# Performance work log

Hardware: AMD Instinct MI355X
Metric: run time of the kernel (lower is better)

The kernel has to match this reference:

```python
import jax, jax.numpy as jnp
import numpy as np

G = 128          # dense grid extent per axis
N = 131072       # number of occupied voxels
MUL = 32         # multiplicity of 0e and 1o irreps
DIM = 4 * MUL    # 32 scalars + 32 vectors*3 = 128
NB = 5           # num_radial_basis
R = 2.5          # diameter / 2
K = 125          # 5^3 kernel offsets


def _lattice_constants():
    # 5x5x5 lattice of physical offsets (steps = 1.0)
    v = jnp.arange(-2.0, 3.0)
    xx, yy, zz = jnp.meshgrid(v, v, v, indexing='ij')
    lattice = jnp.stack([xx, yy, zz], -1)              # (5,5,5,3)
    norm = jnp.linalg.norm(lattice, axis=-1)           # (5,5,5)
    # soft_one_hot_linspace, basis='smooth_finite', cutoff=True
    values = jnp.linspace(0.0, R, NB + 2)[1:-1]
    step = R / (NB + 1)
    d = (norm[..., None] - values) / step              # (5,5,5,NB)
    inside = jnp.abs(d) < 1.0
    ds = jnp.clip(d, -1.0 + 1e-6, 1.0 - 1e-6)
    emb = jnp.where(inside, 1.14136 * jnp.exp(2.0 - 1.0 / (1.0 + ds) - 1.0 / (1.0 - ds)), 0.0)
    # spherical harmonics l=0,1, normalize=True, 'component' norm (e3nn l=1 order: y,z,x)
    unit = jnp.where(norm[..., None] > 0, lattice / jnp.maximum(norm, 1e-9)[..., None], 0.0)
    Y0 = jnp.ones_like(norm)
    Y1 = jnp.sqrt(3.0) * unit[..., (1, 2, 0)]          # (5,5,5,3)
    return emb, Y0, Y1


def _kernel(weight):
    """Generate the (125, DIM, DIM) equivariant kernel (tp.right analogue)."""
    emb, Y0, Y1 = _lattice_constants()
    w = (emb @ weight) / K                              # (5,5,5,4096), /= 5*5*5
    w = w.reshape(5, 5, 5, 4, MUL, MUL)
    Wa, Wb, Wc, Wd = w[..., 0, :, :], w[..., 1, :, :], w[..., 2, :, :], w[..., 3, :, :]
    c = 1.0 / jnp.sqrt(64.0)   # path norm: fan = 2 paths * 32*1 per output
    # 0e x 0e -> 0e
    Kss = c * Wa * Y0[..., None, None]                                        # (...,u,w)
    # 0e x 1o -> 1o  (w3j 1/sqrt3 * sqrt(dim_out=3) = 1)
    Ksv = c * jnp.einsum('...uw,...k->...uwk', Wb, Y1).reshape(5, 5, 5, MUL, 3 * MUL)
    # 1o x 1o -> 0e  (dot / sqrt3)
    Kvs = (c / jnp.sqrt(3.0)) * jnp.einsum('...uw,...i->...uiw', Wd, Y1).reshape(5, 5, 5, 3 * MUL, MUL)
    # 1o x 0e -> 1o  (identity on the 3-vector)
    Kvv = c * jnp.einsum('...uw,ik->...uiwk', Wc * Y0[..., None, None], jnp.eye(3)).reshape(5, 5, 5, 3 * MUL, 3 * MUL)
    kern = jnp.concatenate([jnp.concatenate([Kss, Ksv], -1),
                            jnp.concatenate([Kvs, Kvv], -1)], -2)             # (5,5,5,DIM,DIM)
    kern = jnp.einsum('xyzij->zyxij', kern).reshape(-1, DIM, DIM)             # (125,DIM,DIM)
    return kern


def setup_inputs() -> dict:
    rng = np.random.default_rng(0)
    flat = rng.choice(G ** 3, size=N, replace=False)
    coords = np.stack([flat // (G * G), (flat // G) % G, flat % G], -1).astype(np.int32)
    lookup = np.full(G ** 3, N, np.int32)
    lookup[flat] = np.arange(N, dtype=np.int32)
    # kernel offsets ordered to match the zyx-flattened kernel (x fastest)
    v = np.arange(-2, 3, dtype=np.int32)
    zz, yy, xx = np.meshgrid(v, v, v, indexing='ij')
    offs = np.stack([xx, yy, zz], -1).reshape(-1, 3)                          # (125,3)
    nb = coords[None, :, :] + offs[:, None, :]                                # (125,N,3)
    valid = ((nb >= 0) & (nb < G)).all(-1)
    nf = (nb[..., 0].astype(np.int64) * G + nb[..., 1]) * G + nb[..., 2]
    nf = np.clip(nf, 0, G ** 3 - 1)
    neighbor_idx = np.where(valid, lookup[nf], N).astype(np.int32)            # N = sentinel row

    key = jax.random.key(0)
    k1, k2, k3, k4 = jax.random.split(key, 4)
    return {
        'x_feat': jax.random.normal(k1, (N, DIM), jnp.float32),
        'weight': jax.random.normal(k2, (NB, 4 * MUL * MUL), jnp.float32),
        'w_sc_scal': jax.random.normal(k3, (MUL, MUL), jnp.float32),
        'w_sc_vec': jax.random.normal(k4, (MUL, MUL), jnp.float32),
        'neighbor_idx': jnp.asarray(neighbor_idx),
    }


def reference(x_feat, weight, w_sc_scal, w_sc_vec, neighbor_idx):
    kern = _kernel(weight)                                                    # (125,DIM,DIM)
    # self-connection: equivariant Linear (blockwise, fan_in = MUL)
    inv = 1.0 / jnp.sqrt(jnp.asarray(MUL, x_feat.dtype))
    sc_s = (x_feat[:, :MUL] @ w_sc_scal) * inv
    xv = x_feat[:, MUL:].reshape(-1, MUL, 3)
    sc_v = jnp.einsum('nui,uw->nwi', xv, w_sc_vec).reshape(-1, 3 * MUL) * inv
    sc = jnp.concatenate([sc_s, sc_v], -1)
    # sparse Minkowski conv: gather neighbor rows, matmul per offset, accumulate
    Fp = jnp.concatenate([x_feat, jnp.zeros((1, DIM), x_feat.dtype)], 0)      # sentinel zero row
    def step(acc, kx):
        km, idx = kx
        return acc + Fp[idx] @ km, None
    out, _ = jax.lax.scan(step, jnp.zeros_like(x_feat), (kern, neighbor_idx))
    return sc + out
```

## Files before the change

### kernel.cpp

```cpp
#include <hip/hip_runtime.h>

typedef __attribute__((ext_vector_type(8))) short short8;
typedef __attribute__((ext_vector_type(4))) float f32x4;

#define NPTS 131072
#define NOFF 125
#define KTILE 8192
#define KERN_USH (NOFF * KTILE)

__device__ int g_isf32[4];
__device__ __align__(16) unsigned short g_x[NPTS * 128 + 128];
__device__ __align__(16) unsigned short g_kern[KERN_USH + 128];

__device__ __forceinline__ float bf2f(unsigned short u) {
  unsigned int v = ((unsigned int)u) << 16;
  return __builtin_bit_cast(float, v);
}
__device__ __forceinline__ unsigned short f2bf(float f) {
  unsigned int x = __builtin_bit_cast(unsigned int, f);
  x += 0x7fffu + ((x >> 16) & 1u);
  return (unsigned short)(x >> 16);
}
__device__ __forceinline__ float rdf(const void* p, int i, int isf32) {
  return isf32 ? ((const float*)p)[i] : bf2f(((const unsigned short*)p)[i]);
}

#define GLD16(gp, lp)                                                        \
  __builtin_amdgcn_global_load_lds(                                          \
      (const __attribute__((address_space(1))) unsigned int*)(gp),           \
      (__attribute__((address_space(3))) unsigned int*)(lp), 16, 0, 0)

__global__ __launch_bounds__(64) void k_detect(const unsigned short* x,
                                               const unsigned short* w,
                                               const unsigned short* s,
                                               const unsigned short* v) {
  const unsigned short* ptrs[4] = {x, w, s, v};
  const int l = threadIdx.x;
  #pragma unroll
  for (int i = 0; i < 4; ++i) {
    const unsigned short u = ptrs[i][2 * l];
    const float a = fabsf(bf2f(u));
    const int good = (u == 0) || (a >= 1e-8f && a <= 64.0f);
    const unsigned long long m = __ballot(good);
    if (l == 0) g_isf32[i] = (__popcll(m) < 45) ? 1 : 0;
  }
}

__global__ __launch_bounds__(256) void k_convx(const void* xin) {
  const int t = blockIdx.x * 256 + threadIdx.x;
  const int n = t >> 4;
  const int cp0 = (t & 15) * 8;
  const size_t rb = (size_t)n * 128;
  short8 o;
  if (g_isf32[0]) {
    const float* xf = (const float*)xin;
    #pragma unroll
    for (int j = 0; j < 8; ++j) {
      const int cp = cp0 + j;
      const int src = cp < 32 ? cp : 32 + ((cp - 32) & 31) * 3 + ((cp - 32) >> 5);
      o[j] = (short)f2bf(xf[rb + src]);
    }
  } else {
    const unsigned short* xb = (const unsigned short*)xin;
    #pragma unroll
    for (int j = 0; j < 8; ++j) {
      const int cp = cp0 + j;
      const int src = cp < 32 ? cp : 32 + ((cp - 32) & 31) * 3 + ((cp - 32) >> 5);
      o[j] = (short)xb[rb + src];
    }
  }
  *(short8*)(&g_x[rb + cp0]) = o;
}

__global__ __launch_bounds__(256) void gen_kern(const void* __restrict__ weight,
                                                const void* __restrict__ wscs,
                                                const void* __restrict__ wscv) {
  __shared__ float W[4][32][32];
  __shared__ float embs[5];
  const int wf = g_isf32[1], sf = g_isf32[2], vf = g_isf32[3];
  const int koff = blockIdx.x;
  const int tid = threadIdx.x;
  const int xi = koff % 5, yi = (koff / 5) % 5, zi = koff / 25;
  const float lx = (float)(xi - 2), ly = (float)(yi - 2), lz = (float)(zi - 2);
  const float nrm = sqrtf(lx*lx + ly*ly + lz*lz);
  if (tid < 5) {
    const float step = 2.5f / 6.0f;
    const float vb = step * (float)(tid + 1);
    const float d = (nrm - vb) / step;
    float e = 0.0f;
    if (fabsf(d) < 1.0f) {
      float ds = fminf(fmaxf(d, -1.0f + 1e-6f), 1.0f - 1e-6f);
      e = 1.14136f * expf(2.0f - 1.0f/(1.0f + ds) - 1.0f/(1.0f - ds));
    }
    embs[tid] = e;
  }
  __syncthreads();
  float* Wf = &W[0][0][0];
  for (int m = tid; m < 4096; m += 256) {
    float s = 0.0f;
    #pragma unroll
    for (int b = 0; b < 5; ++b) s += embs[b] * rdf(weight, b*4096 + m, wf);
    Wf[m] = s * (1.0f / 125.0f);
  }
  __syncthreads();
  const float invn = (nrm > 0.0f) ? 1.0f / nrm : 0.0f;
  const float s3 = 1.7320508075688772f;
  const float Y1v0 = s3 * ly * invn;
  const float Y1v1 = s3 * lz * invn;
  const float Y1v2 = s3 * lx * invn;
  const float c  = 0.125f;
  const float cs = 0.125f / s3;
  const bool center = (koff == 62);
  const float inv = 0.17677669529663687f;
  for (int p = tid; p < KTILE; p += 256) {
    const int t = p & 7;
    const int lane = (p >> 3) & 63;
    const int blk = p >> 9;
    const int u = ((lane >> 4) << 3) + t;
    const int w = (blk & 1) * 16 + (lane & 15);
    float val;
    if (blk < 8) {
      const int kb = blk >> 1;
      if (kb == 0) {
        val = c * W[0][u][w];
        if (center) val += inv * rdf(wscs, u*32 + w, sf);
      } else {
        const int i = kb - 1;
        const float y = (i == 0) ? Y1v0 : ((i == 1) ? Y1v1 : Y1v2);
        val = cs * W[3][u][w] * y;
      }
    } else if (blk < 14) {
      const int k = (blk - 8) >> 1;
      const float y = (k == 0) ? Y1v0 : ((k == 1) ? Y1v1 : Y1v2);
      val = c * W[1][u][w] * y;
    } else {
      val = c * W[2][u][w];
      if (center) val += inv * rdf(wscv, u*32 + w, vf);
    }
    g_kern[koff * KTILE + p] = f2bf(val);
  }
}

__global__ __launch_bounds__(512, 4) void conv_main(
    const int* __restrict__ nidx,
    void* __restrict__ out)
{
  __shared__ __align__(16) unsigned short Buf[32768];
  const int of32 = g_isf32[0];
  const char* xb = (const char*)g_x;
  const int tid = threadIdx.x;
  const int wv = tid >> 6;
  const int l  = tid & 63;
  const int lr = l & 15;
  const int lk = l >> 4;
  const int m0 = blockIdx.x * 256 + wv * 32;

  f32x4 acc[2][8];
  #pragma unroll
  for (int i = 0; i < 2; ++i)
    #pragma unroll
    for (int j = 0; j < 8; ++j) acc[i][j] = (f32x4)0.0f;

  {
    const unsigned short* s = g_kern + tid*8;
    short8 p[4];
    #pragma unroll
    for (int c = 0; c < 4; ++c) p[c] = *(const short8*)(s + c*4096);
    #pragma unroll
    for (int c = 0; c < 4; ++c) *(short8*)(&Buf[tid*8 + c*4096]) = p[c];
  }

  bool actc[2];
  int iK1[2], iK2[2], iK3[2];
  short8 a[4][2];
  {
    const int* ip = nidx + m0;
    #pragma unroll
    for (int mt = 0; mt < 2; ++mt) {
      const int idx = __builtin_nontemporal_load(ip + mt*16 + lr);
      const bool vl = (unsigned)idx < (unsigned)NPTS;
      actc[mt] = __any(vl);
      const unsigned uo = (unsigned)idx * 256u + (unsigned)lk * 16u;
      #pragma unroll
      for (int kb = 0; kb < 4; ++kb) {
        short8 v = (short8)(short)0;
        if (vl) v = *(const short8*)(xb + uo + kb*64);
        a[kb][mt] = v;
      }
    }
    const int* ip1 = nidx + (size_t)NPTS + m0;
    #pragma unroll
    for (int mt = 0; mt < 2; ++mt)
      iK1[mt] = __builtin_nontemporal_load(ip1 + mt*16 + lr);
  }
  __syncthreads();

#define KO_SECTION(BB, RIDX, DOREF)                                           \
  {                                                                           \
    const unsigned short* B = &Buf[(BB)];                                     \
    bool vln[2]; bool actn[2]; unsigned uoffn[2];                             \
    if (DOREF) {                                                              \
      _Pragma("unroll")                                                       \
      for (int mt = 0; mt < 2; ++mt) {                                        \
        vln[mt]  = (unsigned)(RIDX)[mt] < (unsigned)NPTS;                     \
        actn[mt] = __any(vln[mt]);                                            \
        uoffn[mt] = (unsigned)(RIDX)[mt] * 256u + (unsigned)lk * 16u;         \
      }                                                                       \
    }                                                                         \
    const bool anyact = actc[0] || actc[1];                                   \
    if (anyact) {                                                             \
      _Pragma("unroll")                                                       \
      for (int kb = 0; kb < 4; ++kb) {                                        \
        const short8 bs0 = *(const short8*)(&B[((kb*2 + 0)*64 + l)*8]);       \
        const short8 bs1 = *(const short8*)(&B[((kb*2 + 1)*64 + l)*8]);       \
        _Pragma("unroll")                                                     \
        for (int mt = 0; mt < 2; ++mt) {                                      \
          if (actc[mt]) {                                                     \
            acc[mt][0] = __builtin_amdgcn_mfma_f32_16x16x32_bf16(             \
                a[kb][mt], bs0, acc[mt][0], 0, 0, 0);                         \
            acc[mt][1] = __builtin_amdgcn_mfma_f32_16x16x32_bf16(             \
                a[kb][mt], bs1, acc[mt][1], 0, 0, 0);                         \
          }                                                                   \
        }                                                                     \
      }                                                                       \
      _Pragma("unroll")                                                       \
      for (int i = 0; i < 3; ++i) {                                           \
        const short8 bsv0 = *(const short8*)(&B[((8 + i*2)*64 + l)*8]);       \
        const short8 bsv1 = *(const short8*)(&B[((9 + i*2)*64 + l)*8]);       \
        _Pragma("unroll")                                                     \
        for (int mt = 0; mt < 2; ++mt) {                                      \
          if (actc[mt]) {                                                     \
            acc[mt][2 + 2*i] = __builtin_amdgcn_mfma_f32_16x16x32_bf16(       \
                a[0][mt], bsv0, acc[mt][2 + 2*i], 0, 0, 0);                   \
            acc[mt][3 + 2*i] = __builtin_amdgcn_mfma_f32_16x16x32_bf16(       \
                a[0][mt], bsv1, acc[mt][3 + 2*i], 0, 0, 0);                   \
          }                                                                   \
        }                                                                     \
      }                                                                       \
    }                                                                         \
    if (DOREF) {                         \
      _Pragma("unroll")                                                       \
      for (int mt = 0; mt < 2; ++mt) {                                        \
        short8 v = (short8)(short)0;                                          \
        if (vln[mt]) v = *(const short8*)(xb + uoffn[mt]);                    \
        a[0][mt] = v;                                                         \
      }                                                                       \
    }                                                                         \
    {                                                                         \
      const short8 bv0 = anyact ? *(const short8*)(&B[(14*64 + l)*8])         \
                                : (short8)(short)0;                           \
      const short8 bv1 = anyact ? *(const short8*)(&B[(15*64 + l)*8])         \
                                : (short8)(short)0;                           \
      _Pragma("unroll")                                                       \
      for (int i = 0; i < 3; ++i) {                                           \
        if (anyact) {                                                         \
          _Pragma("unroll")                                                   \
          for (int mt = 0; mt < 2; ++mt) {                                    \
            if (actc[mt]) {                                                   \
              acc[mt][2 + 2*i] = __builtin_amdgcn_mfma_f32_16x16x32_bf16(     \
                  a[1 + i][mt], bv0, acc[mt][2 + 2*i], 0, 0, 0);              \
              acc[mt][3 + 2*i] = __builtin_amdgcn_mfma_f32_16x16x32_bf16(     \
                  a[1 + i][mt], bv1, acc[mt][3 + 2*i], 0, 0, 0);              \
            }                                                                 \
          }                                                                   \
        }                                                                     \
        if (DOREF) {                  \
          _Pragma("unroll")                                                   \
          for (int mt = 0; mt < 2; ++mt) {                                    \
            short8 v = (short8)(short)0;                                      \
            if (vln[mt]) v = *(const short8*)(xb + uoffn[mt] + (1 + i)*64);   \
            a[1 + i][mt] = v;                                                 \
          }                                                                   \
        }                                                                     \
      }                                                                       \
    }                                                                         \
    if (DOREF) {                                                              \
      _Pragma("unroll")                                                       \
      for (int mt = 0; mt < 2; ++mt) actc[mt] = actn[mt];                     \
    }                                                                         \
  }

  for (int j = 0; j < 62; ++j) {
    const int cur = j & 1;
    const int sb  = (cur ^ 1) * 16384;
    const bool h3 = (j < 61);

    {
      const unsigned short* s0 = g_kern + (size_t)(2*j + 2) * KTILE;
      GLD16(s0 + wv*512 + l*8,        &Buf[sb + wv*512]);
      GLD16(s0 + 4096 + wv*512 + l*8, &Buf[sb + 4096 + wv*512]);
      if (h3) {
        const unsigned short* s1 = g_kern + (size_t)(2*j + 3) * KTILE;
        GLD16(s1 + wv*512 + l*8,        &Buf[sb + 8192 + wv*512]);
        GLD16(s1 + 4096 + wv*512 + l*8, &Buf[sb + 12288 + wv*512]);
      }
    }
    {
      const int* ip2 = nidx + (size_t)(2*j + 2) * NPTS + m0;
      #pragma unroll
      for (int mt = 0; mt < 2; ++mt)
        iK2[mt] = __builtin_nontemporal_load(ip2 + mt*16 + lr);
      if (h3) {
        const int* ip3 = nidx + (size_t)(2*j + 3) * NPTS + m0;
        #pragma unroll
        for (int mt = 0; mt < 2; ++mt)
          iK3[mt] = __builtin_nontemporal_load(ip3 + mt*16 + lr);
      }
    }

    KO_SECTION(cur * 16384,        iK1, true)
    KO_SECTION(cur * 16384 + 8192, iK2, true)

    #pragma unroll
    for (int mt = 0; mt < 2; ++mt) iK1[mt] = iK3[mt];
    __syncthreads();
  }

  KO_SECTION(0, iK1, false)
  __syncthreads();

#undef KO_SECTION

  if (of32) {
    float* of = (float*)out;
    #pragma unroll
    for (int mt = 0; mt < 2; ++mt)
      #pragma unroll
      for (int q = 0; q < 8; ++q) {
        const int oc = (q < 2) ? (q*16 + lr)
                               : 32 + (((q - 2) & 1)*16 + lr)*3 + ((q - 2) >> 1);
        #pragma unroll
        for (int r = 0; r < 4; ++r)
          __builtin_nontemporal_store(
              acc[mt][q][r],
              &of[(size_t)(m0 + mt*16 + lk*4 + r) * 128 + oc]);
      }
  } else {
    unsigned short* eb = &Buf[0];
    #pragma unroll
    for (int mt = 0; mt < 2; ++mt)
      #pragma unroll
      for (int q = 0; q < 8; ++q) {
        const int oc = (q < 2) ? (q*16 + lr)
                               : 32 + (((q - 2) & 1)*16 + lr)*3 + ((q - 2) >> 1);
        #pragma unroll
        for (int r = 0; r < 4; ++r) {
          const int row = wv*32 + mt*16 + lk*4 + r;
          eb[row*128 + (oc ^ ((row & 7) << 3))] = f2bf(acc[mt][q][r]);
        }
      }
    __syncthreads();
    unsigned short* ob = (unsigned short*)out;
    const int row = tid >> 1;
    #pragma unroll
    for (int it = 0; it < 8; ++it) {
      const int ub = (tid & 1)*64 + it*8;
      const short8 v = *(const short8*)(&eb[row*128 + (ub ^ ((row & 7) << 3))]);
      __builtin_nontemporal_store(
          v, (short8*)&ob[(size_t)(blockIdx.x*256 + row) * 128 + ub]);
    }
  }
}

extern "C" void kernel_launch(void* const* d_in, const int* in_sizes, int n_in,
                              void* d_out, int out_size, void* d_ws, size_t ws_size,
                              hipStream_t stream) {
  const void* weight = d_in[1];
  const void* wscs   = d_in[2];
  const void* wscv   = d_in[3];
  const int*  nidx   = (const int*)d_in[4];

  hipLaunchKernelGGL(k_detect, dim3(1), dim3(64), 0, stream,
                     (const unsigned short*)d_in[0], (const unsigned short*)d_in[1],
                     (const unsigned short*)d_in[2], (const unsigned short*)d_in[3]);
  hipLaunchKernelGGL(k_convx, dim3(NPTS * 128 / (256 * 8)), dim3(256), 0, stream, d_in[0]);
  hipLaunchKernelGGL(gen_kern, dim3(NOFF), dim3(256), 0, stream, weight, wscs, wscv);
  hipLaunchKernelGGL(conv_main, dim3(NPTS / 256), dim3(512), 0, stream,
                     nidx, d_out);
}
```

Baseline: 243.2 us.

## Factor vector-to-scalar kernel block via on-the-fly Y-weighted input combination

The 1o→0e block used to be stored as three Y-scaled copies of Wd per offset. Now only one unscaled copy is stored. At runtime each lane combines the three vector components of its gathered input with the per-offset Y values, then issues 2 MFMAs instead of 6. The per-offset kernel tile shrinks from 8192 to 6144 bf16, which cuts LDS and global traffic for kernel staging and lowers MFMA count. In exchange it adds per-element ALU work (bf16 unpack, FMA, repack), an extra bf16 rounding of the combined input, and per-offset global reads of the Y values.

```diff
diff --git a/kernel.cpp b/kernel.cpp
--- a/kernel.cpp
+++ b/kernel.cpp
@@ -5,12 +5,13 @@
 
 #define NPTS 131072
 #define NOFF 125
-#define KTILE 8192
+#define KTILE 6144
 #define KERN_USH (NOFF * KTILE)
 
 __device__ int g_isf32[4];
 __device__ __align__(16) unsigned short g_x[NPTS * 128 + 128];
 __device__ __align__(16) unsigned short g_kern[KERN_USH + 128];
+__device__ __align__(16) float g_y[NOFF][4];
 
 __device__ __forceinline__ float bf2f(unsigned short u) {
   unsigned int v = ((unsigned int)u) << 16;
@@ -112,6 +113,9 @@
   const float cs = 0.125f / s3;
   const bool center = (koff == 62);
   const float inv = 0.17677669529663687f;
+  if (tid == 0) {
+    g_y[koff][0] = Y1v0; g_y[koff][1] = Y1v1; g_y[koff][2] = Y1v2; g_y[koff][3] = 0.0f;
+  }
   for (int p = tid; p < KTILE; p += 256) {
     const int t = p & 7;
     const int lane = (p >> 3) & 63;
@@ -119,18 +123,13 @@
     const int u = ((lane >> 4) << 3) + t;
     const int w = (blk & 1) * 16 + (lane & 15);
     float val;
-    if (blk < 8) {
-      const int kb = blk >> 1;
-      if (kb == 0) {
-        val = c * W[0][u][w];
-        if (center) val += inv * rdf(wscs, u*32 + w, sf);
-      } else {
-        const int i = kb - 1;
-        const float y = (i == 0) ? Y1v0 : ((i == 1) ? Y1v1 : Y1v2);
-        val = cs * W[3][u][w] * y;
-      }
-    } else if (blk < 14) {
-      const int k = (blk - 8) >> 1;
+    if (blk < 2) {
+      val = c * W[0][u][w];
+      if (center) val += inv * rdf(wscs, u*32 + w, sf);
+    } else if (blk < 4) {
+      val = cs * W[3][u][w];
+    } else if (blk < 10) {
+      const int k = (blk - 4) >> 1;
       const float y = (k == 0) ? Y1v0 : ((k == 1) ? Y1v1 : Y1v2);
       val = c * W[1][u][w] * y;
     } else {
@@ -163,11 +162,11 @@
 
   {
     const unsigned short* s = g_kern + tid*8;
-    short8 p[4];
-    #pragma unroll
-    for (int c = 0; c < 4; ++c) p[c] = *(const short8*)(s + c*4096);
-    #pragma unroll
-    for (int c = 0; c < 4; ++c) *(short8*)(&Buf[tid*8 + c*4096]) = p[c];
+    short8 p[3];
+    #pragma unroll
+    for (int c = 0; c < 3; ++c) p[c] = *(const short8*)(s + c*4096);
+    #pragma unroll
+    for (int c = 0; c < 3; ++c) *(short8*)(&Buf[tid*8 + c*4096]) = p[c];
   }
 
   bool actc[2];
@@ -195,9 +194,10 @@
   }
   __syncthreads();
 
-#define KO_SECTION(BB, RIDX, DOREF)                                           \
+#define KO_SECTION(BB, KOY, RIDX, DOREF)                                      \
   {                                                                           \
     const unsigned short* B = &Buf[(BB)];                                     \
+    const float y0 = g_y[(KOY)][0], y1 = g_y[(KOY)][1], y2 = g_y[(KOY)][2];   \
     bool vln[2]; bool actn[2]; unsigned uoffn[2];                             \
     if (DOREF) {                                                              \
       _Pragma("unroll")                                                       \
@@ -209,24 +209,25 @@
     }                                                                         \
     const bool anyact = actc[0] || actc[1];                                   \
     if (anyact) {                                                             \
-      _Pragma("unroll")                                                       \
-      for (int kb = 0; kb < 4; ++kb) {                                        \
-        const short8 bs0 = *(const short8*)(&B[((kb*2 + 0)*64 + l)*8]);       \
-        const short8 bs1 = *(const short8*)(&B[((kb*2 + 1)*64 + l)*8]);       \
+                                                     \
+      {                                                                       \
+        const short8 bs0 = *(const short8*)(&B[((0)*64 + l)*8]);              \
+        const short8 bs1 = *(const short8*)(&B[((1)*64 + l)*8]);              \
         _Pragma("unroll")                                                     \
         for (int mt = 0; mt < 2; ++mt) {                                      \
           if (actc[mt]) {                                                     \
             acc[mt][0] = __builtin_amdgcn_mfma_f32_16x16x32_bf16(             \
-                a[kb][mt], bs0, acc[mt][0], 0, 0, 0);                         \
+                a[0][mt], bs0, acc[mt][0], 0, 0, 0);                          \
             acc[mt][1] = __builtin_amdgcn_mfma_f32_16x16x32_bf16(             \
-                a[kb][mt], bs1, acc[mt][1], 0, 0, 0);                         \
+                a[0][mt], bs1, acc[mt][1], 0, 0, 0);                          \
           }                                                                   \
         }                                                                     \
       }                                                                       \
+                                            \
       _Pragma("unroll")                                                       \
       for (int i = 0; i < 3; ++i) {                                           \
-        const short8 bsv0 = *(const short8*)(&B[((8 + i*2)*64 + l)*8]);       \
-        const short8 bsv1 = *(const short8*)(&B[((9 + i*2)*64 + l)*8]);       \
+        const short8 bsv0 = *(const short8*)(&B[((4 + i*2)*64 + l)*8]);       \
+        const short8 bsv1 = *(const short8*)(&B[((5 + i*2)*64 + l)*8]);       \
         _Pragma("unroll")                                                     \
         for (int mt = 0; mt < 2; ++mt) {                                      \
           if (actc[mt]) {                                                     \
@@ -246,10 +247,32 @@
         a[0][mt] = v;                                                         \
       }                                                                       \
     }                                                                         \
+    if (anyact) {                                                             \
+                    \
+      const short8 bw0 = *(const short8*)(&B[((2)*64 + l)*8]);                \
+      const short8 bw1 = *(const short8*)(&B[((3)*64 + l)*8]);                \
+      _Pragma("unroll")                                                       \
+      for (int mt = 0; mt < 2; ++mt) {                                        \
+        if (actc[mt]) {                                                       \
+          short8 xvY;                                                         \
+          _Pragma("unroll")                                                   \
+          for (int jj = 0; jj < 8; ++jj) {                                    \
+            const float f = y0 * bf2f((unsigned short)a[1][mt][jj])           \
+                          + y1 * bf2f((unsigned short)a[2][mt][jj])           \
+                          + y2 * bf2f((unsigned short)a[3][mt][jj]);          \
+            xvY[jj] = (short)f2bf(f);                                         \
+          }                                                                   \
+          acc[mt][0] = __builtin_amdgcn_mfma_f32_16x16x32_bf16(               \
+              xvY, bw0, acc[mt][0], 0, 0, 0);                                 \
+          acc[mt][1] = __builtin_amdgcn_mfma_f32_16x16x32_bf16(               \
+              xvY, bw1, acc[mt][1], 0, 0, 0);                                 \
+        }                                                                     \
+      }                                                                       \
+    }                                                                         \
     {                                                                         \
-      const short8 bv0 = anyact ? *(const short8*)(&B[(14*64 + l)*8])         \
+      const short8 bv0 = anyact ? *(const short8*)(&B[(10*64 + l)*8])         \
                                 : (short8)(short)0;                           \
-      const short8 bv1 = anyact ? *(const short8*)(&B[(15*64 + l)*8])         \
+      const short8 bv1 = anyact ? *(const short8*)(&B[(11*64 + l)*8])         \
                                 : (short8)(short)0;                           \
       _Pragma("unroll")                                                       \
       for (int i = 0; i < 3; ++i) {                                           \
@@ -281,19 +304,19 @@
   }
 
   for (int j = 0; j < 62; ++j) {
-    const int cur = j & 1;
-    const int sb  = (cur ^ 1) * 16384;
+    const int cur = (j & 1) * 12288;
+    const int sb  = 12288 - cur;
     const bool h3 = (j < 61);
 
-    {
+    if (h3) {
       const unsigned short* s0 = g_kern + (size_t)(2*j + 2) * KTILE;
-      GLD16(s0 + wv*512 + l*8,        &Buf[sb + wv*512]);
-      GLD16(s0 + 4096 + wv*512 + l*8, &Buf[sb + 4096 + wv*512]);
-      if (h3) {
-        const unsigned short* s1 = g_kern + (size_t)(2*j + 3) * KTILE;
-        GLD16(s1 + wv*512 + l*8,        &Buf[sb + 8192 + wv*512]);
-        GLD16(s1 + 4096 + wv*512 + l*8, &Buf[sb + 12288 + wv*512]);
-      }
+      #pragma unroll
+      for (int c = 0; c < 3; ++c)
+        GLD16(s0 + c*4096 + wv*512 + l*8, &Buf[sb + c*4096 + wv*512]);
+    } else {
+      const unsigned short* s0 = g_kern + (size_t)124 * KTILE;
+      GLD16(s0 + wv*512 + l*8, &Buf[sb + wv*512]);
+      if (wv < 4) GLD16(s0 + 4096 + wv*512 + l*8, &Buf[sb + 4096 + wv*512]);
     }
     {
       const int* ip2 = nidx + (size_t)(2*j + 2) * NPTS + m0;
@@ -308,15 +331,15 @@
       }
     }
 
-    KO_SECTION(cur * 16384,        iK1, true)
-    KO_SECTION(cur * 16384 + 8192, iK2, true)
+    KO_SECTION(cur,        2*j,     iK1, true)
+    KO_SECTION(cur + 6144, 2*j + 1, iK2, true)
 
     #pragma unroll
     for (int mt = 0; mt < 2; ++mt) iK1[mt] = iK3[mt];
     __syncthreads();
   }
 
-  KO_SECTION(0, iK1, false)
+  KO_SECTION(0, 124, iK1, false)
   __syncthreads();
 
 #undef KO_SECTION
```

Result: slower. 669.2 us (+175.2%).
